# Kernel tuning notes

Hardware: AMD Instinct MI355X
Metric: run time of the kernel (lower is better)

Reference implementation:

```python
import jax, jax.numpy as jnp
import numpy as np

ALPHA_1 = 0.5
ALPHA_2 = 0.9
TAU = 0.1
BIG_NUM = 1.0e9


def setup_inputs() -> dict:
    key = jax.random.key(0)
    k1, k2 = jax.random.split(key)
    B, N_SUP, N_QRY, D = 4, 512, 4096, 128
    features = jax.random.normal(k1, (B, N_SUP + N_QRY, D), dtype=jnp.float32)
    support_labels = jax.random.randint(k2, (B, N_SUP), 0, 64, dtype=jnp.int64)
    return {"features": features, "support_labels": support_labels}


def _sq_dists(x, y):
    # squared Euclidean pairwise distances: [B, N, M]
    xn = jnp.sum(x * x, axis=-1)  # [B, N]
    yn = jnp.sum(y * y, axis=-1)  # [B, M]
    xy = jnp.einsum('bnd,bmd->bnm', x, y)
    return xn[:, :, None] + yn[:, None, :] - 2.0 * xy


def reference(features, support_labels):
    n_support = support_labels.shape[1]
    support = features[:, :n_support]   # [B, S, D]
    query = features[:, n_support:]     # [B, Q, D]

    # --- re_represent_queries ---
    logits = -TAU * _sq_dists(query, query)           # [B, Q, Q]
    Q = query.shape[1]
    rng = jnp.arange(Q)
    logits = logits.at[:, rng, rng].set(-BIG_NUM)     # mask self-similarity
    attn_q = jax.nn.softmax(logits, axis=2)
    # Faithful to source: (attn[:,:,:,None] * q[:,:,None,:]).sum(2)
    # i.e. row index of q matches row index of attn; softmax axis j is contracted
    # against a broadcast copy of the same row.
    re_rep_q = jnp.einsum('bij,bid->bid', attn_q, query)
    new_query = (1.0 - ALPHA_1) * query + ALPHA_1 * re_rep_q

    # --- re_represent_supports ---
    logits_s = -TAU * _sq_dists(support, new_query)   # [B, S, Q]
    attn_s = jax.nn.softmax(logits_s, axis=2)
    re_rep_s = jnp.einsum('bsq,bqd->bsd', attn_s, new_query)
    new_support = (1.0 - ALPHA_2) * support + ALPHA_2 * re_rep_s

    return jnp.concatenate((new_support, new_query), axis=1)
```

## Files before the change

### kernel.cpp

```cpp
#include <hip/hip_runtime.h>

#define BATCH 4
#define NS 512
#define NQ 4096
#define D 128
#define NTOT (NS + NQ)

#define NCHUNK 16
#define QCHUNK (NQ / NCHUNK)
#define QT 64
#define ST 64
#define PITN 136
#define PITT 72

typedef __attribute__((ext_vector_type(8))) short bf16x8;
typedef __attribute__((ext_vector_type(4))) float f32x4;

#define L2E 1.4426950408889634f

__device__ __forceinline__ unsigned short f2bf(float f) {
    unsigned int x = __float_as_uint(f);
    return (unsigned short)((x + 0x7fffu + ((x >> 16) & 1u)) >> 16);
}

__global__ __launch_bounds__(256) void prep_kernel(const float* __restrict__ feat,
                                                   float* __restrict__ out,
                                                   float* __restrict__ qnl) {
    int wave = threadIdx.x >> 6;
    int lane = threadIdx.x & 63;
    int row = blockIdx.x * 4 + wave;
    int b = row >> 12;
    int q = row & (NQ - 1);
    size_t off = ((size_t)b * NTOT + NS + q) * D + lane * 2;
    float2 v = *(const float2*)(feat + off);
    *(float2*)(out + off) = v;
    float s = v.x * v.x + v.y * v.y;
    #pragma unroll
    for (int w = 32; w >= 1; w >>= 1) s += __shfl_down(s, w, 64);
    if (lane == 0) qnl[row] = 0.1f * L2E * s;
}

__global__ __launch_bounds__(256) void attend_kernel(const float* __restrict__ feat,
                                                     const float* __restrict__ qnl,
                                                     float* __restrict__ acc,
                                                     float* __restrict__ lsum) {
    __shared__ unsigned short qn_[QT * PITN];
    __shared__ unsigned short qt_[D * PITT];
    __shared__ unsigned short p_[ST * PITT];
    __shared__ float qns[QCHUNK];

    int chunk = blockIdx.x, stile = blockIdx.y, b = blockIdx.z;
    int s0 = stile * ST;
    int q0 = chunk * QCHUNK;
    int t = threadIdx.x;
    int w = t >> 6;
    int ln = t & 15;
    int quad = (t >> 4) & 3;

    qns[t] = qnl[b * NQ + q0 + t];

    const float* srow = feat + ((size_t)b * NTOT + s0 + 16 * w + ln) * D;
    bf16x8 asup[4];
    #pragma unroll
    for (int kk = 0; kk < 4; ++kk) {
        float4 lo = *(const float4*)(srow + 32 * kk + 8 * quad);
        float4 hi = *(const float4*)(srow + 32 * kk + 8 * quad + 4);
        union { bf16x8 v; unsigned short u[8]; } pk;
        pk.u[0] = f2bf(lo.x); pk.u[1] = f2bf(lo.y); pk.u[2] = f2bf(lo.z); pk.u[3] = f2bf(lo.w);
        pk.u[4] = f2bf(hi.x); pk.u[5] = f2bf(hi.y); pk.u[6] = f2bf(hi.z); pk.u[7] = f2bf(hi.w);
        asup[kk] = pk.v;
    }

    f32x4 cpv[8];
    #pragma unroll
    for (int ds = 0; ds < 8; ++ds) cpv[ds] = (f32x4){0.f, 0.f, 0.f, 0.f};
    float lpart[4] = {0.f, 0.f, 0.f, 0.f};

    int qrow = t >> 2;
    int dgrp = (t & 3) * 4;

    const float* qchunk_base = feat + ((size_t)b * NTOT + NS + q0) * D;

    for (int qt = 0; qt < QCHUNK; qt += QT) {
        __syncthreads();
        const float* qbase = qchunk_base + (size_t)(qt + qrow) * D;
        #pragma unroll
        for (int i = 0; i < 8; ++i) {
            int d = dgrp + 16 * i;
            float4 v = *(const float4*)(qbase + d);
            unsigned short b0 = f2bf(v.x), b1 = f2bf(v.y), b2 = f2bf(v.z), b3 = f2bf(v.w);
            unsigned int w0 = (unsigned int)b0 | ((unsigned int)b1 << 16);
            unsigned int w1 = (unsigned int)b2 | ((unsigned int)b3 << 16);
            *(unsigned int*)&qn_[qrow * PITN + d]     = w0;
            *(unsigned int*)&qn_[qrow * PITN + d + 2] = w1;
            qt_[(d + 0) * PITT + qrow] = b0;
            qt_[(d + 1) * PITT + qrow] = b1;
            qt_[(d + 2) * PITT + qrow] = b2;
            qt_[(d + 3) * PITT + qrow] = b3;
        }
        __syncthreads();

        f32x4 cqk[4];
        #pragma unroll
        for (int f = 0; f < 4; ++f) cqk[f] = (f32x4){0.f, 0.f, 0.f, 0.f};
        #pragma unroll
        for (int kk = 0; kk < 4; ++kk) {
            #pragma unroll
            for (int f = 0; f < 4; ++f) {
                bf16x8 bq = *(const bf16x8*)&qn_[(16 * f + ln) * PITN + 32 * kk + 8 * quad];
                cqk[f] = __builtin_amdgcn_mfma_f32_16x16x32_bf16(asup[kk], bq, cqk[f], 0, 0, 0);
            }
        }

        #pragma unroll
        for (int f = 0; f < 4; ++f) {
            float qs = qns[qt + 16 * f + ln];
            #pragma unroll
            for (int r = 0; r < 4; ++r) {
                float e = exp2f(0.2f * L2E * cqk[f][r] - qs);
                lpart[r] += e;
                p_[(16 * w + 4 * quad + r) * PITT + 16 * f + ln] = f2bf(e);
            }
        }
        __syncthreads();

        #pragma unroll
        for (int kk = 0; kk < 2; ++kk) {
            bf16x8 ap = *(const bf16x8*)&p_[(16 * w + ln) * PITT + 32 * kk + 8 * quad];
            #pragma unroll
            for (int ds = 0; ds < 8; ++ds) {
                bf16x8 bv = *(const bf16x8*)&qt_[(16 * ds + ln) * PITT + 32 * kk + 8 * quad];
                cpv[ds] = __builtin_amdgcn_mfma_f32_16x16x32_bf16(ap, bv, cpv[ds], 0, 0, 0);
            }
        }
    }

    #pragma unroll
    for (int r = 0; r < 4; ++r) {
        float v = lpart[r];
        v += __shfl_xor(v, 1, 64);
        v += __shfl_xor(v, 2, 64);
        v += __shfl_xor(v, 4, 64);
        v += __shfl_xor(v, 8, 64);
        if (ln == 0) atomicAdd(&lsum[b * NS + s0 + 16 * w + 4 * quad + r], v);
    }
    #pragma unroll
    for (int ds = 0; ds < 8; ++ds)
        #pragma unroll
        for (int r = 0; r < 4; ++r)
            atomicAdd(&acc[((size_t)b * NS + s0 + 16 * w + 4 * quad + r) * D + 16 * ds + ln],
                      cpv[ds][r]);
}

__global__ __launch_bounds__(256) void epi_kernel(const float* __restrict__ feat,
                                                  const float* __restrict__ acc,
                                                  const float* __restrict__ lsum,
                                                  float* __restrict__ out) {
    int wave = threadIdx.x >> 6;
    int lane = threadIdx.x & 63;
    int row = blockIdx.x * 4 + wave;
    int b = row >> 9;
    int s = row & (NS - 1);
    float inv = 0.9f / lsum[row];
    size_t fo = ((size_t)b * NTOT + s) * D + lane * 2;
    float2 sup = *(const float2*)(feat + fo);
    float2 a = *(const float2*)(acc + (size_t)row * D + lane * 2);
    float2 o;
    o.x = 0.1f * sup.x + a.x * inv;
    o.y = 0.1f * sup.y + a.y * inv;
    *(float2*)(out + fo) = o;
}

extern "C" void kernel_launch(void* const* d_in, const int* in_sizes, int n_in,
                              void* d_out, int out_size, void* d_ws, size_t ws_size,
                              hipStream_t stream) {
    const float* feat = (const float*)d_in[0];
    float* out = (float*)d_out;
    float* ws = (float*)d_ws;
    float* qnl  = ws;
    float* acc  = ws + BATCH * NQ;
    float* lsum = acc + BATCH * NS * D;
    (void)in_sizes; (void)n_in; (void)out_size; (void)ws_size;

    hipMemsetAsync(acc, 0, (size_t)(BATCH * NS * D + BATCH * NS) * sizeof(float), stream);
    prep_kernel<<<BATCH * NQ / 4, 256, 0, stream>>>(feat, out, qnl);
    attend_kernel<<<dim3(NCHUNK, NS / ST, BATCH), 256, 0, stream>>>(feat, qnl, acc, lsum);
    epi_kernel<<<BATCH * NS / 4, 256, 0, stream>>>(feat, acc, lsum, out);
}
```

Measured before the change: 99.38 us.

## Precompute bf16 query and transposed copies in prep, enlarge support tile

The prep kernel now converts the queries to bf16 once and writes both a row-major copy and a transposed copy to workspace. The attention kernel then loads ready bf16 tiles with wide copies, instead of converting fp32 and scattering transposed stores into shared memory in every block. Each block now covers 128 supports (two M sub-tiles that share the B operands) and the query range is split into 32 chunks, so register use rises. The extra workspace traffic and the larger accumulator footprint are the cost.

New measurement: 113.5 us. 14.2% more time.

```diff
diff --git a/kernel.cpp b/kernel.cpp
--- a/kernel.cpp
+++ b/kernel.cpp
@@ -6,10 +6,10 @@
 #define D 128
 #define NTOT (NS + NQ)
 
-#define NCHUNK 16
+#define NCHUNK 32
 #define QCHUNK (NQ / NCHUNK)
 #define QT 64
-#define ST 64
+#define ST 128
 #define PITN 136
 #define PITT 72
 
@@ -17,6 +17,7 @@
 typedef __attribute__((ext_vector_type(4))) float f32x4;
 
 #define L2E 1.4426950408889634f
+#define SCL 0.28853900817779268f
 
 __device__ __forceinline__ unsigned short f2bf(float f) {
     unsigned int x = __float_as_uint(f);
@@ -25,25 +26,55 @@
 
 __global__ __launch_bounds__(256) void prep_kernel(const float* __restrict__ feat,
                                                    float* __restrict__ out,
-                                                   float* __restrict__ qnl) {
-    int wave = threadIdx.x >> 6;
-    int lane = threadIdx.x & 63;
-    int row = blockIdx.x * 4 + wave;
-    int b = row >> 12;
-    int q = row & (NQ - 1);
-    size_t off = ((size_t)b * NTOT + NS + q) * D + lane * 2;
-    float2 v = *(const float2*)(feat + off);
-    *(float2*)(out + off) = v;
-    float s = v.x * v.x + v.y * v.y;
-    #pragma unroll
-    for (int w = 32; w >= 1; w >>= 1) s += __shfl_down(s, w, 64);
-    if (lane == 0) qnl[row] = 0.1f * L2E * s;
-}
-
-__global__ __launch_bounds__(256) void attend_kernel(const float* __restrict__ feat,
-                                                     const float* __restrict__ qnl,
-                                                     float* __restrict__ acc,
-                                                     float* __restrict__ lsum) {
+                                                   float* __restrict__ qnl,
+                                                   unsigned short* __restrict__ Qb,
+                                                   unsigned short* __restrict__ QTb) {
+    __shared__ unsigned short lt[QT][PITN];
+    int b = blockIdx.y;
+    int q0 = blockIdx.x * QT;
+    int t = threadIdx.x;
+    int row = t >> 2;
+    int cg = (t & 3) * 32;
+    const float* src = feat + ((size_t)b * NTOT + NS + q0 + row) * D + cg;
+    float* dst = out + ((size_t)b * NTOT + NS + q0 + row) * D + cg;
+    unsigned short* qb = Qb + ((size_t)b * NQ + q0 + row) * D + cg;
+    float nrm = 0.f;
+    #pragma unroll
+    for (int i = 0; i < 8; ++i) {
+        float4 v = *(const float4*)(src + 4 * i);
+        *(float4*)(dst + 4 * i) = v;
+        nrm += v.x * v.x + v.y * v.y + v.z * v.z + v.w * v.w;
+        unsigned short b0 = f2bf(v.x), b1 = f2bf(v.y), b2 = f2bf(v.z), b3 = f2bf(v.w);
+        uint2 pk = make_uint2((unsigned)b0 | ((unsigned)b1 << 16),
+                              (unsigned)b2 | ((unsigned)b3 << 16));
+        *(uint2*)(qb + 4 * i) = pk;
+        *(uint2*)&lt[row][cg + 4 * i] = pk;
+    }
+    nrm += __shfl_xor(nrm, 1, 64);
+    nrm += __shfl_xor(nrm, 2, 64);
+    if ((t & 3) == 0) qnl[b * NQ + q0 + row] = 0.1f * L2E * nrm;
+    __syncthreads();
+    int d = t >> 1;
+    int qs = (t & 1) * 32;
+    unsigned int wbuf[16];
+    #pragma unroll
+    for (int j = 0; j < 16; ++j) {
+        unsigned short a = lt[qs + 2 * j][d];
+        unsigned short c = lt[qs + 2 * j + 1][d];
+        wbuf[j] = (unsigned)a | ((unsigned)c << 16);
+    }
+    unsigned short* qt = QTb + ((size_t)b * D + d) * NQ + q0 + qs;
+    #pragma unroll
+    for (int j = 0; j < 4; ++j)
+        *(uint4*)(qt + 8 * j) = make_uint4(wbuf[4*j], wbuf[4*j+1], wbuf[4*j+2], wbuf[4*j+3]);
+}
+
+__global__ __launch_bounds__(256, 2) void attend_kernel(const float* __restrict__ feat,
+                                                        const unsigned short* __restrict__ Qb,
+                                                        const unsigned short* __restrict__ QTb,
+                                                        const float* __restrict__ qnl,
+                                                        float* __restrict__ acc,
+                                                        float* __restrict__ lsum) {
     __shared__ unsigned short qn_[QT * PITN];
     __shared__ unsigned short qt_[D * PITT];
     __shared__ unsigned short p_[ST * PITT];
@@ -53,103 +84,118 @@
     int s0 = stile * ST;
     int q0 = chunk * QCHUNK;
     int t = threadIdx.x;
-    int w = t >> 6;
-    int ln = t & 15;
-    int quad = (t >> 4) & 3;
-
-    qns[t] = qnl[b * NQ + q0 + t];
-
-    const float* srow = feat + ((size_t)b * NTOT + s0 + 16 * w + ln) * D;
-    bf16x8 asup[4];
-    #pragma unroll
-    for (int kk = 0; kk < 4; ++kk) {
-        float4 lo = *(const float4*)(srow + 32 * kk + 8 * quad);
-        float4 hi = *(const float4*)(srow + 32 * kk + 8 * quad + 4);
-        union { bf16x8 v; unsigned short u[8]; } pk;
-        pk.u[0] = f2bf(lo.x); pk.u[1] = f2bf(lo.y); pk.u[2] = f2bf(lo.z); pk.u[3] = f2bf(lo.w);
-        pk.u[4] = f2bf(hi.x); pk.u[5] = f2bf(hi.y); pk.u[6] = f2bf(hi.z); pk.u[7] = f2bf(hi.w);
-        asup[kk] = pk.v;
-    }
-
-    f32x4 cpv[8];
-    #pragma unroll
-    for (int ds = 0; ds < 8; ++ds) cpv[ds] = (f32x4){0.f, 0.f, 0.f, 0.f};
-    float lpart[4] = {0.f, 0.f, 0.f, 0.f};
-
-    int qrow = t >> 2;
-    int dgrp = (t & 3) * 4;
-
-    const float* qchunk_base = feat + ((size_t)b * NTOT + NS + q0) * D;
+    int w = t >> 6, ln = t & 15, quad = (t >> 4) & 3;
+
+    if (t < QCHUNK) qns[t] = qnl[b * NQ + q0 + t];
+
+    bf16x8 asup[2][4];
+    #pragma unroll
+    for (int mt = 0; mt < 2; ++mt) {
+        const float* srow = feat + ((size_t)b * NTOT + s0 + 64 * mt + 16 * w + ln) * D;
+        #pragma unroll
+        for (int kk = 0; kk < 4; ++kk) {
+            float4 lo = *(const float4*)(srow + 32 * kk + 8 * quad);
+            float4 hi = *(const float4*)(srow + 32 * kk + 8 * quad + 4);
+            union { bf16x8 v; unsigned short u[8]; } pk;
+            pk.u[0] = f2bf(lo.x); pk.u[1] = f2bf(lo.y); pk.u[2] = f2bf(lo.z); pk.u[3] = f2bf(lo.w);
+            pk.u[4] = f2bf(hi.x); pk.u[5] = f2bf(hi.y); pk.u[6] = f2bf(hi.z); pk.u[7] = f2bf(hi.w);
+            asup[mt][kk] = pk.v;
+        }
+    }
+
+    f32x4 cpv[2][8];
+    #pragma unroll
+    for (int mt = 0; mt < 2; ++mt)
+        #pragma unroll
+        for (int ds = 0; ds < 8; ++ds) cpv[mt][ds] = (f32x4){0.f, 0.f, 0.f, 0.f};
+    float lpart[2][4] = {{0.f,0.f,0.f,0.f},{0.f,0.f,0.f,0.f}};
+
+    int srw = t >> 2, sseg = (t & 3) * 32;
+    int drw = t >> 1, dseg = (t & 1) * 32;
 
     for (int qt = 0; qt < QCHUNK; qt += QT) {
         __syncthreads();
-        const float* qbase = qchunk_base + (size_t)(qt + qrow) * D;
-        #pragma unroll
-        for (int i = 0; i < 8; ++i) {
-            int d = dgrp + 16 * i;
-            float4 v = *(const float4*)(qbase + d);
-            unsigned short b0 = f2bf(v.x), b1 = f2bf(v.y), b2 = f2bf(v.z), b3 = f2bf(v.w);
-            unsigned int w0 = (unsigned int)b0 | ((unsigned int)b1 << 16);
-            unsigned int w1 = (unsigned int)b2 | ((unsigned int)b3 << 16);
-            *(unsigned int*)&qn_[qrow * PITN + d]     = w0;
-            *(unsigned int*)&qn_[qrow * PITN + d + 2] = w1;
-            qt_[(d + 0) * PITT + qrow] = b0;
-            qt_[(d + 1) * PITT + qrow] = b1;
-            qt_[(d + 2) * PITT + qrow] = b2;
-            qt_[(d + 3) * PITT + qrow] = b3;
-        }
+        const unsigned short* qsrc = Qb + ((size_t)b * NQ + q0 + qt + srw) * D + sseg;
+        const unsigned short* tsrc = QTb + ((size_t)b * D + drw) * NQ + q0 + qt + dseg;
+        #pragma unroll
+        for (int i = 0; i < 4; ++i)
+            *(uint4*)&qn_[srw * PITN + sseg + 8 * i] = *(const uint4*)(qsrc + 8 * i);
+        #pragma unroll
+        for (int i = 0; i < 4; ++i)
+            *(uint4*)&qt_[drw * PITT + dseg + 8 * i] = *(const uint4*)(tsrc + 8 * i);
         __syncthreads();
 
-        f32x4 cqk[4];
-        #pragma unroll
-        for (int f = 0; f < 4; ++f) cqk[f] = (f32x4){0.f, 0.f, 0.f, 0.f};
+        f32x4 cqk[2][4];
+        #pragma unroll
+        for (int mt = 0; mt < 2; ++mt)
+            #pragma unroll
+            for (int f = 0; f < 4; ++f) cqk[mt][f] = (f32x4){0.f, 0.f, 0.f, 0.f};
         #pragma unroll
         for (int kk = 0; kk < 4; ++kk) {
+            bf16x8 bq[4];
+            #pragma unroll
+            for (int f = 0; f < 4; ++f)
+                bq[f] = *(const bf16x8*)&qn_[(16 * f + ln) * PITN + 32 * kk + 8 * quad];
+            #pragma unroll
+            for (int mt = 0; mt < 2; ++mt)
+                #pragma unroll
+                for (int f = 0; f < 4; ++f)
+                    cqk[mt][f] = __builtin_amdgcn_mfma_f32_16x16x32_bf16(asup[mt][kk], bq[f],
+                                                                         cqk[mt][f], 0, 0, 0);
+        }
+
+        #pragma unroll
+        for (int mt = 0; mt < 2; ++mt)
             #pragma unroll
             for (int f = 0; f < 4; ++f) {
-                bf16x8 bq = *(const bf16x8*)&qn_[(16 * f + ln) * PITN + 32 * kk + 8 * quad];
-                cqk[f] = __builtin_amdgcn_mfma_f32_16x16x32_bf16(asup[kk], bq, cqk[f], 0, 0, 0);
+                float qs = qns[qt + 16 * f + ln];
+                #pragma unroll
+                for (int r = 0; r < 4; ++r) {
+                    float e = exp2f(SCL * cqk[mt][f][r] - qs);
+                    lpart[mt][r] += e;
+                    p_[(16 * w + 64 * mt + 4 * quad + r) * PITT + 16 * f + ln] = f2bf(e);
+                }
             }
-        }
-
-        #pragma unroll
-        for (int f = 0; f < 4; ++f) {
-            float qs = qns[qt + 16 * f + ln];
-            #pragma unroll
-            for (int r = 0; r < 4; ++r) {
-                float e = exp2f(0.2f * L2E * cqk[f][r] - qs);
-                lpart[r] += e;
-                p_[(16 * w + 4 * quad + r) * PITT + 16 * f + ln] = f2bf(e);
-            }
-        }
         __syncthreads();
 
         #pragma unroll
         for (int kk = 0; kk < 2; ++kk) {
-            bf16x8 ap = *(const bf16x8*)&p_[(16 * w + ln) * PITT + 32 * kk + 8 * quad];
+            bf16x8 ap[2];
+            #pragma unroll
+            for (int mt = 0; mt < 2; ++mt)
+                ap[mt] = *(const bf16x8*)&p_[(16 * w + 64 * mt + ln) * PITT + 32 * kk + 8 * quad];
             #pragma unroll
             for (int ds = 0; ds < 8; ++ds) {
                 bf16x8 bv = *(const bf16x8*)&qt_[(16 * ds + ln) * PITT + 32 * kk + 8 * quad];
-                cpv[ds] = __builtin_amdgcn_mfma_f32_16x16x32_bf16(ap, bv, cpv[ds], 0, 0, 0);
+                #pragma unroll
+                for (int mt = 0; mt < 2; ++mt)
+                    cpv[mt][ds] = __builtin_amdgcn_mfma_f32_16x16x32_bf16(ap[mt], bv,
+                                                                          cpv[mt][ds], 0, 0, 0);
             }
         }
     }
 
     #pragma unroll
-    for (int r = 0; r < 4; ++r) {
-        float v = lpart[r];
-        v += __shfl_xor(v, 1, 64);
-        v += __shfl_xor(v, 2, 64);
-        v += __shfl_xor(v, 4, 64);
-        v += __shfl_xor(v, 8, 64);
-        if (ln == 0) atomicAdd(&lsum[b * NS + s0 + 16 * w + 4 * quad + r], v);
-    }
-    #pragma unroll
-    for (int ds = 0; ds < 8; ++ds)
-        #pragma unroll
-        for (int r = 0; r < 4; ++r)
-            atomicAdd(&acc[((size_t)b * NS + s0 + 16 * w + 4 * quad + r) * D + 16 * ds + ln],
-                      cpv[ds][r]);
+    for (int mt = 0; mt < 2; ++mt)
+        #pragma unroll
+        for (int r = 0; r < 4; ++r) {
+            float v = lpart[mt][r];
+            v += __shfl_xor(v, 1, 64);
+            v += __shfl_xor(v, 2, 64);
+            v += __shfl_xor(v, 4, 64);
+            v += __shfl_xor(v, 8, 64);
+            if (ln == 0)
+                atomicAdd(&lsum[b * NS + s0 + 16 * w + 64 * mt + 4 * quad + r], v);
+        }
+    #pragma unroll
+    for (int mt = 0; mt < 2; ++mt)
+        #pragma unroll
+        for (int ds = 0; ds < 8; ++ds)
+            #pragma unroll
+            for (int r = 0; r < 4; ++r)
+                atomicAdd(&acc[((size_t)b * NS + s0 + 16 * w + 64 * mt + 4 * quad + r) * D
+                               + 16 * ds + ln],
+                          cpv[mt][ds][r]);
 }
 
 __global__ __launch_bounds__(256) void epi_kernel(const float* __restrict__ feat,
@@ -177,13 +223,15 @@
     const float* feat = (const float*)d_in[0];
     float* out = (float*)d_out;
     float* ws = (float*)d_ws;
-    float* qnl  = ws;
-    float* acc  = ws + BATCH * NQ;
+    float* acc  = ws;
     float* lsum = acc + BATCH * NS * D;
+    float* qnl  = lsum + BATCH * NS;
+    unsigned short* Qb  = (unsigned short*)(qnl + BATCH * NQ);
+    unsigned short* QTb = Qb + (size_t)BATCH * NQ * D;
     (void)in_sizes; (void)n_in; (void)out_size; (void)ws_size;
 
     hipMemsetAsync(acc, 0, (size_t)(BATCH * NS * D + BATCH * NS) * sizeof(float), stream);
-    prep_kernel<<<BATCH * NQ / 4, 256, 0, stream>>>(feat, out, qnl);
-    attend_kernel<<<dim3(NCHUNK, NS / ST, BATCH), 256, 0, stream>>>(feat, qnl, acc, lsum);
+    prep_kernel<<<dim3(NQ / QT, BATCH), 256, 0, stream>>>(feat, out, qnl, Qb, QTb);
+    attend_kernel<<<dim3(NCHUNK, NS / ST, BATCH), 256, 0, stream>>>(feat, Qb, QTb, qnl, acc, lsum);
     epi_kernel<<<BATCH * NS / 4, 256, 0, stream>>>(feat, acc, lsum, out);
 }
```

## Precompute bf16 query and transposed copies to simplify attend tile loads

Applied to the files above, without the earlier changes.

The prep stage now writes a bf16 copy of the queries and a separate kernel writes a transposed bf16 copy. The attend kernel then fills its shared-memory tiles with 16-byte vector copies instead of converting fp32 to bf16 and doing scattered 2-byte transposed stores on every tile. This removes conversion work and LDS bank conflicts that were repeated across all 8 support tiles. In exchange it adds an extra kernel launch and a global write/read round trip for two bf16 copies of the queries.

Result: slower. 102.6 us (+3.3%).

```diff
diff --git a/kernel.cpp b/kernel.cpp
--- a/kernel.cpp
+++ b/kernel.cpp
@@ -17,15 +17,17 @@
 typedef __attribute__((ext_vector_type(4))) float f32x4;
 
 #define L2E 1.4426950408889634f
+#define SCL 0.28853900817779268f
 
 __device__ __forceinline__ unsigned short f2bf(float f) {
     unsigned int x = __float_as_uint(f);
     return (unsigned short)((x + 0x7fffu + ((x >> 16) & 1u)) >> 16);
 }
 
-__global__ __launch_bounds__(256) void prep_kernel(const float* __restrict__ feat,
-                                                   float* __restrict__ out,
-                                                   float* __restrict__ qnl) {
+__global__ __launch_bounds__(256) void prep1_kernel(const float* __restrict__ feat,
+                                                    float* __restrict__ out,
+                                                    float* __restrict__ qnl,
+                                                    unsigned short* __restrict__ Qb) {
     int wave = threadIdx.x >> 6;
     int lane = threadIdx.x & 63;
     int row = blockIdx.x * 4 + wave;
@@ -34,13 +36,41 @@
     size_t off = ((size_t)b * NTOT + NS + q) * D + lane * 2;
     float2 v = *(const float2*)(feat + off);
     *(float2*)(out + off) = v;
+    *(unsigned int*)(Qb + ((size_t)b * NQ + q) * D + lane * 2) =
+        (unsigned)f2bf(v.x) | ((unsigned)f2bf(v.y) << 16);
     float s = v.x * v.x + v.y * v.y;
     #pragma unroll
     for (int w = 32; w >= 1; w >>= 1) s += __shfl_down(s, w, 64);
     if (lane == 0) qnl[row] = 0.1f * L2E * s;
 }
 
+__global__ __launch_bounds__(256) void prep2_kernel(const unsigned short* __restrict__ Qb,
+                                                    unsigned short* __restrict__ QTb) {
+    __shared__ unsigned short lt[64][72];
+    int q0 = blockIdx.x * 64, d0 = blockIdx.y * 64, b = blockIdx.z;
+    int t = threadIdx.x;
+    #pragma unroll
+    for (int k = 0; k < 2; ++k) {
+        int idx = t + k * 256;
+        int q = idx >> 3, ds = (idx & 7) * 8;
+        *(uint4*)&lt[q][ds] = *(const uint4*)&Qb[((size_t)b * NQ + q0 + q) * D + d0 + ds];
+    }
+    __syncthreads();
+    #pragma unroll
+    for (int k = 0; k < 2; ++k) {
+        int idx = t + k * 256;
+        int d = idx >> 3, qs = (idx & 7) * 8;
+        unsigned int w0 = (unsigned)lt[qs + 0][d] | ((unsigned)lt[qs + 1][d] << 16);
+        unsigned int w1 = (unsigned)lt[qs + 2][d] | ((unsigned)lt[qs + 3][d] << 16);
+        unsigned int w2 = (unsigned)lt[qs + 4][d] | ((unsigned)lt[qs + 5][d] << 16);
+        unsigned int w3 = (unsigned)lt[qs + 6][d] | ((unsigned)lt[qs + 7][d] << 16);
+        *(uint4*)&QTb[((size_t)b * D + d0 + d) * NQ + q0 + qs] = make_uint4(w0, w1, w2, w3);
+    }
+}
+
 __global__ __launch_bounds__(256) void attend_kernel(const float* __restrict__ feat,
+                                                     const unsigned short* __restrict__ Qb,
+                                                     const unsigned short* __restrict__ QTb,
                                                      const float* __restrict__ qnl,
                                                      float* __restrict__ acc,
                                                      float* __restrict__ lsum) {
@@ -53,9 +83,7 @@
     int s0 = stile * ST;
     int q0 = chunk * QCHUNK;
     int t = threadIdx.x;
-    int w = t >> 6;
-    int ln = t & 15;
-    int quad = (t >> 4) & 3;
+    int w = t >> 6, ln = t & 15, quad = (t >> 4) & 3;
 
     qns[t] = qnl[b * NQ + q0 + t];
 
@@ -76,28 +104,19 @@
     for (int ds = 0; ds < 8; ++ds) cpv[ds] = (f32x4){0.f, 0.f, 0.f, 0.f};
     float lpart[4] = {0.f, 0.f, 0.f, 0.f};
 
-    int qrow = t >> 2;
-    int dgrp = (t & 3) * 4;
-
-    const float* qchunk_base = feat + ((size_t)b * NTOT + NS + q0) * D;
+    int srw = t >> 2, sseg = (t & 3) * 32;
+    int drw = t >> 1, dseg = (t & 1) * 32;
 
     for (int qt = 0; qt < QCHUNK; qt += QT) {
         __syncthreads();
-        const float* qbase = qchunk_base + (size_t)(qt + qrow) * D;
-        #pragma unroll
-        for (int i = 0; i < 8; ++i) {
-            int d = dgrp + 16 * i;
-            float4 v = *(const float4*)(qbase + d);
-            unsigned short b0 = f2bf(v.x), b1 = f2bf(v.y), b2 = f2bf(v.z), b3 = f2bf(v.w);
-            unsigned int w0 = (unsigned int)b0 | ((unsigned int)b1 << 16);
-            unsigned int w1 = (unsigned int)b2 | ((unsigned int)b3 << 16);
-            *(unsigned int*)&qn_[qrow * PITN + d]     = w0;
-            *(unsigned int*)&qn_[qrow * PITN + d + 2] = w1;
-            qt_[(d + 0) * PITT + qrow] = b0;
-            qt_[(d + 1) * PITT + qrow] = b1;
-            qt_[(d + 2) * PITT + qrow] = b2;
-            qt_[(d + 3) * PITT + qrow] = b3;
-        }
+        const unsigned short* qsrc = Qb + ((size_t)b * NQ + q0 + qt + srw) * D + sseg;
+        const unsigned short* tsrc = QTb + ((size_t)b * D + drw) * NQ + q0 + qt + dseg;
+        #pragma unroll
+        for (int i = 0; i < 4; ++i)
+            *(uint4*)&qn_[srw * PITN + sseg + 8 * i] = *(const uint4*)(qsrc + 8 * i);
+        #pragma unroll
+        for (int i = 0; i < 4; ++i)
+            *(uint4*)&qt_[drw * PITT + dseg + 8 * i] = *(const uint4*)(tsrc + 8 * i);
         __syncthreads();
 
         f32x4 cqk[4];
@@ -117,7 +136,7 @@
             float qs = qns[qt + 16 * f + ln];
             #pragma unroll
             for (int r = 0; r < 4; ++r) {
-                float e = exp2f(0.2f * L2E * cqk[f][r] - qs);
+                float e = exp2f(SCL * cqk[f][r] - qs);
                 lpart[r] += e;
                 p_[(16 * w + 4 * quad + r) * PITT + 16 * f + ln] = f2bf(e);
             }
@@ -177,13 +196,16 @@
     const float* feat = (const float*)d_in[0];
     float* out = (float*)d_out;
     float* ws = (float*)d_ws;
-    float* qnl  = ws;
-    float* acc  = ws + BATCH * NQ;
+    float* acc  = ws;
     float* lsum = acc + BATCH * NS * D;
+    float* qnl  = lsum + BATCH * NS;
+    unsigned short* Qb  = (unsigned short*)(qnl + BATCH * NQ);
+    unsigned short* QTb = Qb + (size_t)BATCH * NQ * D;
     (void)in_sizes; (void)n_in; (void)out_size; (void)ws_size;
 
     hipMemsetAsync(acc, 0, (size_t)(BATCH * NS * D + BATCH * NS) * sizeof(float), stream);
-    prep_kernel<<<BATCH * NQ / 4, 256, 0, stream>>>(feat, out, qnl);
-    attend_kernel<<<dim3(NCHUNK, NS / ST, BATCH), 256, 0, stream>>>(feat, qnl, acc, lsum);
+    prep1_kernel<<<BATCH * NQ / 4, 256, 0, stream>>>(feat, out, qnl, Qb);
+    prep2_kernel<<<dim3(NQ / 64, D / 64, BATCH), 256, 0, stream>>>(Qb, QTb);
+    attend_kernel<<<dim3(NCHUNK, NS / ST, BATCH), 256, 0, stream>>>(feat, Qb, QTb, qnl, acc, lsum);
     epi_kernel<<<BATCH * NS / 4, 256, 0, stream>>>(feat, acc, lsum, out);
 }
```

## Fuse query-norm prep into attend and replace atomics with per-chunk partials

Applied to the files above, without the earlier changes.

Removes the separate prep kernel by computing query squared norms inside the attend kernel and distributing the query passthrough copy across blocks. Replaces the global atomicAdd accumulation and the memset with per-chunk partial buffers, which the epilogue sums. This cuts two launches and the atomic contention. In exchange it adds a larger workspace footprint and extra epilogue reads.

Result: faster. 85.64 us (-13.8%).

```diff
diff --git a/kernel.cpp b/kernel.cpp
--- a/kernel.cpp
+++ b/kernel.cpp
@@ -17,33 +17,17 @@
 typedef __attribute__((ext_vector_type(4))) float f32x4;
 
 #define L2E 1.4426950408889634f
+#define SCL 0.28853900817779268f
 
 __device__ __forceinline__ unsigned short f2bf(float f) {
     unsigned int x = __float_as_uint(f);
     return (unsigned short)((x + 0x7fffu + ((x >> 16) & 1u)) >> 16);
 }
 
-__global__ __launch_bounds__(256) void prep_kernel(const float* __restrict__ feat,
-                                                   float* __restrict__ out,
-                                                   float* __restrict__ qnl) {
-    int wave = threadIdx.x >> 6;
-    int lane = threadIdx.x & 63;
-    int row = blockIdx.x * 4 + wave;
-    int b = row >> 12;
-    int q = row & (NQ - 1);
-    size_t off = ((size_t)b * NTOT + NS + q) * D + lane * 2;
-    float2 v = *(const float2*)(feat + off);
-    *(float2*)(out + off) = v;
-    float s = v.x * v.x + v.y * v.y;
-    #pragma unroll
-    for (int w = 32; w >= 1; w >>= 1) s += __shfl_down(s, w, 64);
-    if (lane == 0) qnl[row] = 0.1f * L2E * s;
-}
-
 __global__ __launch_bounds__(256) void attend_kernel(const float* __restrict__ feat,
-                                                     const float* __restrict__ qnl,
-                                                     float* __restrict__ acc,
-                                                     float* __restrict__ lsum) {
+                                                     float* __restrict__ out,
+                                                     float* __restrict__ accP,
+                                                     float* __restrict__ lsumP) {
     __shared__ unsigned short qn_[QT * PITN];
     __shared__ unsigned short qt_[D * PITT];
     __shared__ unsigned short p_[ST * PITT];
@@ -53,11 +37,7 @@
     int s0 = stile * ST;
     int q0 = chunk * QCHUNK;
     int t = threadIdx.x;
-    int w = t >> 6;
-    int ln = t & 15;
-    int quad = (t >> 4) & 3;
-
-    qns[t] = qnl[b * NQ + q0 + t];
+    int w = t >> 6, ln = t & 15, quad = (t >> 4) & 3;
 
     const float* srow = feat + ((size_t)b * NTOT + s0 + 16 * w + ln) * D;
     bf16x8 asup[4];
@@ -78,26 +58,33 @@
 
     int qrow = t >> 2;
     int dgrp = (t & 3) * 4;
-
     const float* qchunk_base = feat + ((size_t)b * NTOT + NS + q0) * D;
+    float* outq = out + ((size_t)b * NTOT + NS + q0) * D;
+    int copy_qt = (stile >> 1) << 6;
+    int copy_ok = (qrow >> 5) == (stile & 1);
 
     for (int qt = 0; qt < QCHUNK; qt += QT) {
         __syncthreads();
         const float* qbase = qchunk_base + (size_t)(qt + qrow) * D;
+        float nrm = 0.f;
+        int docopy = (qt == copy_qt) & copy_ok;
         #pragma unroll
         for (int i = 0; i < 8; ++i) {
             int d = dgrp + 16 * i;
             float4 v = *(const float4*)(qbase + d);
+            if (docopy) *(float4*)(outq + (size_t)(qt + qrow) * D + d) = v;
+            nrm += v.x * v.x + v.y * v.y + v.z * v.z + v.w * v.w;
             unsigned short b0 = f2bf(v.x), b1 = f2bf(v.y), b2 = f2bf(v.z), b3 = f2bf(v.w);
-            unsigned int w0 = (unsigned int)b0 | ((unsigned int)b1 << 16);
-            unsigned int w1 = (unsigned int)b2 | ((unsigned int)b3 << 16);
-            *(unsigned int*)&qn_[qrow * PITN + d]     = w0;
-            *(unsigned int*)&qn_[qrow * PITN + d + 2] = w1;
+            *(unsigned int*)&qn_[qrow * PITN + d]     = (unsigned)b0 | ((unsigned)b1 << 16);
+            *(unsigned int*)&qn_[qrow * PITN + d + 2] = (unsigned)b2 | ((unsigned)b3 << 16);
             qt_[(d + 0) * PITT + qrow] = b0;
             qt_[(d + 1) * PITT + qrow] = b1;
             qt_[(d + 2) * PITT + qrow] = b2;
             qt_[(d + 3) * PITT + qrow] = b3;
         }
+        nrm += __shfl_xor(nrm, 1, 64);
+        nrm += __shfl_xor(nrm, 2, 64);
+        if ((t & 3) == 0) qns[qt + qrow] = 0.1f * L2E * nrm;
         __syncthreads();
 
         f32x4 cqk[4];
@@ -117,7 +104,7 @@
             float qs = qns[qt + 16 * f + ln];
             #pragma unroll
             for (int r = 0; r < 4; ++r) {
-                float e = exp2f(0.2f * L2E * cqk[f][r] - qs);
+                float e = exp2f(SCL * cqk[f][r] - qs);
                 lpart[r] += e;
                 p_[(16 * w + 4 * quad + r) * PITT + 16 * f + ln] = f2bf(e);
             }
@@ -135,6 +122,7 @@
         }
     }
 
+    int base = (chunk * BATCH + b) * NS + s0;
     #pragma unroll
     for (int r = 0; r < 4; ++r) {
         float v = lpart[r];
@@ -142,32 +130,39 @@
         v += __shfl_xor(v, 2, 64);
         v += __shfl_xor(v, 4, 64);
         v += __shfl_xor(v, 8, 64);
-        if (ln == 0) atomicAdd(&lsum[b * NS + s0 + 16 * w + 4 * quad + r], v);
+        if (ln == 0) lsumP[base + 16 * w + 4 * quad + r] = v;
     }
     #pragma unroll
     for (int ds = 0; ds < 8; ++ds)
         #pragma unroll
         for (int r = 0; r < 4; ++r)
-            atomicAdd(&acc[((size_t)b * NS + s0 + 16 * w + 4 * quad + r) * D + 16 * ds + ln],
-                      cpv[ds][r]);
+            accP[(size_t)(base + 16 * w + 4 * quad + r) * D + 16 * ds + ln] = cpv[ds][r];
 }
 
 __global__ __launch_bounds__(256) void epi_kernel(const float* __restrict__ feat,
-                                                  const float* __restrict__ acc,
-                                                  const float* __restrict__ lsum,
+                                                  const float* __restrict__ accP,
+                                                  const float* __restrict__ lsumP,
                                                   float* __restrict__ out) {
     int wave = threadIdx.x >> 6;
     int lane = threadIdx.x & 63;
     int row = blockIdx.x * 4 + wave;
     int b = row >> 9;
     int s = row & (NS - 1);
-    float inv = 0.9f / lsum[row];
+
+    float l = 0.f, ax = 0.f, ay = 0.f;
+    #pragma unroll 4
+    for (int c = 0; c < NCHUNK; ++c) {
+        int base = (c * BATCH + b) * NS + s;
+        l += lsumP[base];
+        float2 a = *(const float2*)(accP + (size_t)base * D + lane * 2);
+        ax += a.x; ay += a.y;
+    }
+    float inv = 0.9f / l;
     size_t fo = ((size_t)b * NTOT + s) * D + lane * 2;
     float2 sup = *(const float2*)(feat + fo);
-    float2 a = *(const float2*)(acc + (size_t)row * D + lane * 2);
     float2 o;
-    o.x = 0.1f * sup.x + a.x * inv;
-    o.y = 0.1f * sup.y + a.y * inv;
+    o.x = 0.1f * sup.x + ax * inv;
+    o.y = 0.1f * sup.y + ay * inv;
     *(float2*)(out + fo) = o;
 }
 
@@ -177,13 +172,10 @@
     const float* feat = (const float*)d_in[0];
     float* out = (float*)d_out;
     float* ws = (float*)d_ws;
-    float* qnl  = ws;
-    float* acc  = ws + BATCH * NQ;
-    float* lsum = acc + BATCH * NS * D;
+    float* accP  = ws;
+    float* lsumP = accP + (size_t)NCHUNK * BATCH * NS * D;
     (void)in_sizes; (void)n_in; (void)out_size; (void)ws_size;
 
-    hipMemsetAsync(acc, 0, (size_t)(BATCH * NS * D + BATCH * NS) * sizeof(float), stream);
-    prep_kernel<<<BATCH * NQ / 4, 256, 0, stream>>>(feat, out, qnl);
-    attend_kernel<<<dim3(NCHUNK, NS / ST, BATCH), 256, 0, stream>>>(feat, qnl, acc, lsum);
-    epi_kernel<<<BATCH * NS / 4, 256, 0, stream>>>(feat, acc, lsum, out);
+    attend_kernel<<<dim3(NCHUNK, NS / ST, BATCH), 256, 0, stream>>>(feat, out, accP, lsumP);
+    epi_kernel<<<BATCH * NS / 4, 256, 0, stream>>>(feat, accP, lsumP, out);
 }
```
